# Kernel tuning notes

Hardware: AMD Instinct MI355X
Metric: run time of the kernel (lower is better)

The kernel has to match this reference:

```python
import jax, jax.numpy as jnp
import numpy as np

B, T, D, H = 2, 2048, 1024, 16
DH = D // H  # head_dim = 64
ROPE_BASE = 10000.0


def _rope_cos_sin(seq_len, dh, dtype):
    inv_freq = 1.0 / (ROPE_BASE ** (jnp.arange(0, dh, 2, dtype=jnp.float32) / dh))
    t = jnp.arange(seq_len, dtype=jnp.float32)
    freqs = jnp.outer(t, inv_freq)            # [T, dh/2]
    emb = jnp.concatenate([freqs, freqs], -1)  # [T, dh]
    return jnp.cos(emb).astype(dtype), jnp.sin(emb).astype(dtype)


def _rotate_half(x):
    half = x.shape[-1] // 2
    return jnp.concatenate([-x[..., half:], x[..., :half]], axis=-1)


def setup_inputs() -> dict:
    key = jax.random.key(0)
    k1, k2, k3 = jax.random.split(key, 3)
    x = jax.random.normal(k1, (B, T, D), dtype=jnp.float32)
    w_qkv = jax.random.normal(k2, (D, 3 * D), dtype=jnp.float32) * (D ** -0.5)
    w_out = jax.random.normal(k3, (D, D), dtype=jnp.float32) * (D ** -0.5)
    return {"x": x, "w_qkv": w_qkv, "w_out": w_out}


def reference(x, w_qkv, w_out):
    b, t, _ = x.shape
    qkv = x @ w_qkv                                        # [B,T,3D]
    qkv = qkv.reshape(b, t, 3, H, DH).transpose(2, 0, 3, 1, 4)  # [3,B,H,T,DH]
    q, k, v = qkv[0], qkv[1], qkv[2]

    cos, sin = _rope_cos_sin(t, DH, x.dtype)               # [T,DH] each
    q = q * cos + _rotate_half(q) * sin
    k = k * cos + _rotate_half(k) * sin

    scale = DH ** -0.5
    scores = jnp.einsum('bhtd,bhsd->bhts', q, k) * scale   # [B,H,T,T]
    # dense additive causal mask (as in original module)
    neg = jnp.finfo(x.dtype).min
    causal = jnp.triu(jnp.ones((t, t), dtype=bool), k=1)
    scores = scores + jnp.where(causal, neg, jnp.zeros((), x.dtype))
    attn = jax.nn.softmax(scores, axis=-1)
    out = jnp.einsum('bhts,bhsd->bhtd', attn, v)           # [B,H,T,DH]
    out = out.transpose(0, 2, 1, 3).reshape(b, t, D)       # [B,T,D]
    return out @ w_out
```

## Files before the change

### kernel.cpp

```cpp
#include <hip/hip_runtime.h>

typedef __bf16 bf16x8 __attribute__((ext_vector_type(8)));
typedef float f32x4 __attribute__((ext_vector_type(4)));
typedef unsigned int u32x4 __attribute__((ext_vector_type(4)));
typedef unsigned int u32x2 __attribute__((ext_vector_type(2)));
typedef unsigned short u16;
typedef unsigned int u32;

#define BSZ 2
#define TSEQ 2048
#define DMODEL 1024
#define NHEAD 16
#define DHEAD 64

#define GLDS(gp, lp)                                                        \
  __builtin_amdgcn_global_load_lds(                                         \
      (const __attribute__((address_space(1))) void*)(gp),                  \
      (__attribute__((address_space(3))) void*)(lp), 16, 0, 0)

#define TRR(dst, base, OFF)                                                 \
  asm volatile("ds_read_b64_tr_b16 %0, %1 offset:" OFF                     \
               : "=v"(dst) : "v"(base) : "memory")

__device__ __forceinline__ u16 f2bf(float f) {
  return __builtin_bit_cast(u16, (__bf16)f);
}
__device__ __forceinline__ u32 pack2bf(float lo, float hi) {
  return (u32)f2bf(lo) | ((u32)f2bf(hi) << 16);
}
__device__ __forceinline__ float bf2f(u16 h) {
  return __builtin_bit_cast(float, (u32)h << 16);
}

__global__ void k_prep(const float* __restrict__ x, u16* __restrict__ xb,
                       const float* __restrict__ wqkv, u16* __restrict__ wqkvT,
                       const float* __restrict__ wout, u16* __restrict__ woutT,
                       float* __restrict__ cosT, float* __restrict__ sinT) {
  __shared__ float tile[64][65];
  int blk = blockIdx.x, tid = threadIdx.x;
  if (blk < 2048) {
    int i = blk * 256 + tid;
    const float4* f4 = (const float4*)x;
    float4 v0 = f4[i * 2], v1 = f4[i * 2 + 1];
    u32x4 o;
    o[0] = pack2bf(v0.x, v0.y); o[1] = pack2bf(v0.z, v0.w);
    o[2] = pack2bf(v1.x, v1.y); o[3] = pack2bf(v1.z, v1.w);
    ((u32x4*)xb)[i] = o;
  } else if (blk < 2816) {
    int idx = blk - 2048;
    int n0 = (idx % 48) * 64, k0 = (idx / 48) * 64;
    int tx = tid & 63, ty = tid >> 6;
#pragma unroll
    for (int i = ty; i < 64; i += 4)
      tile[i][tx] = wqkv[(size_t)(k0 + i) * 3072 + n0 + tx];
    __syncthreads();
#pragma unroll
    for (int i = ty; i < 64; i += 4)
      wqkvT[(size_t)(n0 + i) * 1024 + k0 + tx] = f2bf(tile[tx][i]);
  } else if (blk < 3072) {
    int idx = blk - 2816;
    int n0 = (idx % 16) * 64, k0 = (idx / 16) * 64;
    int tx = tid & 63, ty = tid >> 6;
#pragma unroll
    for (int i = ty; i < 64; i += 4)
      tile[i][tx] = wout[(size_t)(k0 + i) * 1024 + n0 + tx];
    __syncthreads();
#pragma unroll
    for (int i = ty; i < 64; i += 4)
      woutT[(size_t)(n0 + i) * 1024 + k0 + tx] = f2bf(tile[tx][i]);
  } else {
    int idx = (blk - 3072) * 256 + tid;
    int t = idx >> 5, f = idx & 31;
    float inv_freq = powf(10000.0f, -(float)(2 * f) / 64.0f);
    float ang = (float)t * inv_freq;
    float s, c;
    sincosf(ang, &s, &c);
    cosT[idx] = c;
    sinT[idx] = s;
  }
}

__global__ __launch_bounds__(256) void k_gemm_qkv(const u16* __restrict__ A,
                                                  const u16* __restrict__ Bt,
                                                  u16* __restrict__ Qh, u16* __restrict__ Kh,
                                                  u16* __restrict__ Vh,
                                                  const float* __restrict__ cosT,
                                                  const float* __restrict__ sinT) {
  const int K = DMODEL;
  __shared__ __align__(16) u16 a_lds[2][128][32];
  __shared__ __align__(16) u16 b_lds[2][128][32];
  int m0 = blockIdx.y * 128, n0 = blockIdx.x * 128;
  int tid = threadIdx.x;
  int w = tid >> 6, l = tid & 63, lr = l & 15, lg = l >> 4;
  int wr = (w >> 1) * 64, wc = (w & 1) * 64;
  int grow = l >> 2;
  int gcol = (l & 3) * 8;
  f32x4 acc[4][4] = {};

  const u16* a0 = A + (size_t)(m0 + w * 16 + grow) * K + gcol;
  const u16* a1 = A + (size_t)(m0 + (w + 4) * 16 + grow) * K + gcol;
  const u16* b0 = Bt + (size_t)(n0 + w * 16 + grow) * K + gcol;
  const u16* b1 = Bt + (size_t)(n0 + (w + 4) * 16 + grow) * K + gcol;

  int NT = K >> 5;
  GLDS(a0, &a_lds[0][w * 16][0]);
  GLDS(a1, &a_lds[0][(w + 4) * 16][0]);
  GLDS(b0, &b_lds[0][w * 16][0]);
  GLDS(b1, &b_lds[0][(w + 4) * 16][0]);

  for (int t = 0; t < NT; ++t) {
    int p = t & 1;
    if (t + 1 < NT) {
      int k0 = (t + 1) << 5;
      GLDS(a0 + k0, &a_lds[p ^ 1][w * 16][0]);
      GLDS(a1 + k0, &a_lds[p ^ 1][(w + 4) * 16][0]);
      GLDS(b0 + k0, &b_lds[p ^ 1][w * 16][0]);
      GLDS(b1 + k0, &b_lds[p ^ 1][(w + 4) * 16][0]);
      asm volatile("s_waitcnt vmcnt(4)" ::: "memory");
    } else {
      asm volatile("s_waitcnt vmcnt(0)" ::: "memory");
    }
    __builtin_amdgcn_s_barrier();
    __builtin_amdgcn_sched_barrier(0);
    bf16x8 af[4], bfv[4];
#pragma unroll
    for (int mt = 0; mt < 4; ++mt)
      af[mt] = __builtin_bit_cast(bf16x8, *(const u32x4*)&a_lds[p][wr + mt * 16 + lr][lg * 8]);
#pragma unroll
    for (int nt = 0; nt < 4; ++nt)
      bfv[nt] = __builtin_bit_cast(bf16x8, *(const u32x4*)&b_lds[p][wc + nt * 16 + lr][lg * 8]);
    __builtin_amdgcn_s_setprio(1);
#pragma unroll
    for (int mt = 0; mt < 4; ++mt)
#pragma unroll
      for (int nt = 0; nt < 4; ++nt)
        acc[mt][nt] = __builtin_amdgcn_mfma_f32_16x16x32_bf16(af[mt], bfv[nt], acc[mt][nt], 0, 0, 0);
    __builtin_amdgcn_s_setprio(0);
    __builtin_amdgcn_sched_barrier(0);
    __builtin_amdgcn_s_barrier();
  }

  int sec = n0 >> 10;
  int hcol = ((n0 + wc) & 1023) >> 6;
  u16* outp = (sec == 0) ? Qh : (sec == 1) ? Kh : Vh;
  float qscale = (sec == 0) ? 0.125f : 1.0f;
#pragma unroll
  for (int mt = 0; mt < 4; ++mt)
#pragma unroll
    for (int r = 0; r < 4; ++r) {
      int row = m0 + wr + mt * 16 + lg * 4 + r;
      int b = row >> 11, tt = row & 2047;
      size_t obase = ((size_t)((b * 16 + hcol) * 2048 + tt)) * 64;
      if (sec == 2) {
#pragma unroll
        for (int nt = 0; nt < 4; ++nt)
          outp[obase + nt * 16 + lr] = f2bf(acc[mt][nt][r]);
      } else {
        float c0 = cosT[tt * 32 + lr],      s0 = sinT[tt * 32 + lr];
        float c1 = cosT[tt * 32 + 16 + lr], s1 = sinT[tt * 32 + 16 + lr];
        float v0 = acc[mt][0][r], v1 = acc[mt][1][r];
        float v2 = acc[mt][2][r], v3 = acc[mt][3][r];
        outp[obase + lr]      = f2bf((v0 * c0 - v2 * s0) * qscale);
        outp[obase + 16 + lr] = f2bf((v1 * c1 - v3 * s1) * qscale);
        outp[obase + 32 + lr] = f2bf((v2 * c0 + v0 * s0) * qscale);
        outp[obase + 48 + lr] = f2bf((v3 * c1 + v1 * s1) * qscale);
      }
    }
}

__global__ __launch_bounds__(256) void k_gemm_out(const u16* __restrict__ A,
                                                  const u16* __restrict__ Bt,
                                                  float* __restrict__ C) {
  const int N = 1024, K = 1024;
  __shared__ __align__(16) u16 a_lds[2][128][32];
  __shared__ __align__(16) u16 b_lds[2][64][32];
  int m0 = blockIdx.y * 128, n0 = blockIdx.x * 64;
  int tid = threadIdx.x;
  int w = tid >> 6, l = tid & 63, lr = l & 15, lg = l >> 4;
  int wr = (w >> 1) * 64, wc = (w & 1) * 32;
  int grow = l >> 2;
  int gcol = (l & 3) * 8;
  f32x4 acc[4][2] = {};

  const u16* a0 = A + (size_t)(m0 + w * 16 + grow) * K + gcol;
  const u16* a1 = A + (size_t)(m0 + (w + 4) * 16 + grow) * K + gcol;
  const u16* b0 = Bt + (size_t)(n0 + w * 16 + grow) * K + gcol;

  int NT = K >> 5;
  GLDS(a0, &a_lds[0][w * 16][0]);
  GLDS(a1, &a_lds[0][(w + 4) * 16][0]);
  GLDS(b0, &b_lds[0][w * 16][0]);

  for (int t = 0; t < NT; ++t) {
    int p = t & 1;
    if (t + 1 < NT) {
      int k0 = (t + 1) << 5;
      GLDS(a0 + k0, &a_lds[p ^ 1][w * 16][0]);
      GLDS(a1 + k0, &a_lds[p ^ 1][(w + 4) * 16][0]);
      GLDS(b0 + k0, &b_lds[p ^ 1][w * 16][0]);
      asm volatile("s_waitcnt vmcnt(3)" ::: "memory");
    } else {
      asm volatile("s_waitcnt vmcnt(0)" ::: "memory");
    }
    __builtin_amdgcn_s_barrier();
    __builtin_amdgcn_sched_barrier(0);
    bf16x8 af[4], bfv[2];
#pragma unroll
    for (int mt = 0; mt < 4; ++mt)
      af[mt] = __builtin_bit_cast(bf16x8, *(const u32x4*)&a_lds[p][wr + mt * 16 + lr][lg * 8]);
#pragma unroll
    for (int nt = 0; nt < 2; ++nt)
      bfv[nt] = __builtin_bit_cast(bf16x8, *(const u32x4*)&b_lds[p][wc + nt * 16 + lr][lg * 8]);
    __builtin_amdgcn_s_setprio(1);
#pragma unroll
    for (int mt = 0; mt < 4; ++mt)
#pragma unroll
      for (int nt = 0; nt < 2; ++nt)
        acc[mt][nt] = __builtin_amdgcn_mfma_f32_16x16x32_bf16(af[mt], bfv[nt], acc[mt][nt], 0, 0, 0);
    __builtin_amdgcn_s_setprio(0);
    __builtin_amdgcn_sched_barrier(0);
    __builtin_amdgcn_s_barrier();
  }

#pragma unroll
  for (int mt = 0; mt < 4; ++mt)
#pragma unroll
    for (int nt = 0; nt < 2; ++nt)
#pragma unroll
      for (int r = 0; r < 4; ++r) {
        int row = m0 + wr + mt * 16 + lg * 4 + r;
        int col = n0 + wc + nt * 16 + lr;
        C[(size_t)row * N + col] = acc[mt][nt][r];
      }
}

__global__ __launch_bounds__(512) void k_flash(const u16* __restrict__ Qg, const u16* __restrict__ Kg,
                                               const u16* __restrict__ Vg, u16* __restrict__ O) {
  __shared__ __align__(16) u16 k_lds[2][64][72];
  __shared__ __align__(16) u16 vsub[2][4096];
  __shared__ __align__(16) u16 p_lds[8][16][68];
  int pp = blockIdx.x;
  int qb1 = 31 - pp, qb2 = pp;
  int bh = blockIdx.y;
  int b = bh >> 4, h = bh & 15;
  size_t hoff = (size_t)bh * TSEQ * DHEAD;
  int tid = threadIdx.x, w = tid >> 6, l = tid & 63, lr = l & 15, lg = l >> 4;
  int team = w >> 2, wt = w & 3;
  int qb_t = team ? qb2 : qb1;

  int srow = tid >> 3;
  int g8 = tid & 7;
  int sc8 = g8 * 8;
  u32 vtr0 = (u32)(uintptr_t)vsub + (u32)(lg * 1024 + lr * 8);

  const u16* kbase = Kg + hoff;
  const u16* vbase = Vg + hoff;

  const u16* qp = Qg + hoff + (size_t)(qb_t * 64 + wt * 16 + lr) * 64 + lg * 8;
  bf16x8 qf0 = __builtin_bit_cast(bf16x8, *(const u32x4*)qp);
  bf16x8 qf1 = __builtin_bit_cast(bf16x8, *(const u32x4*)(qp + 32));

  f32x4 acc[4] = {};
  float mrow[4] = {-1e30f, -1e30f, -1e30f, -1e30f};
  float lsum[4] = {0.f, 0.f, 0.f, 0.f};

  u32x4 kreg, vreg;
  kreg = *(const u32x4*)(kbase + (size_t)srow * 64 + sc8);
  vreg = *(const u32x4*)(vbase + (size_t)srow * 64 + sc8);

  for (int kv = 0; kv <= qb1; ++kv) {
    int cur = kv & 1;
    *(u32x4*)&k_lds[cur][srow][sc8] = kreg;
    int vo = ((srow >> 2) * 4 + (g8 >> 1)) * 64 + (srow & 3) * 16 + (g8 & 1) * 8;
    *(u32x4*)&vsub[cur][vo] = vreg;
    __syncthreads();
    if (kv < qb1) {
      int r = (kv + 1) * 64 + srow;
      kreg = *(const u32x4*)(kbase + (size_t)r * 64 + sc8);
      vreg = *(const u32x4*)(vbase + (size_t)r * 64 + sc8);
    }

    if (kv <= qb_t) {
      u32 vtr = vtr0 + (u32)(cur * 8192);
      f32x4 s[4];
      __builtin_amdgcn_s_setprio(1);
#pragma unroll
      for (int c = 0; c < 4; ++c) {
        const u16* kp2 = &k_lds[cur][c * 16 + lr][lg * 8];
        bf16x8 kf0 = __builtin_bit_cast(bf16x8, *(const u32x4*)kp2);
        bf16x8 kf1 = __builtin_bit_cast(bf16x8, *(const u32x4*)(kp2 + 32));
        f32x4 z = {};
        z = __builtin_amdgcn_mfma_f32_16x16x32_bf16(qf0, kf0, z, 0, 0, 0);
        s[c] = __builtin_amdgcn_mfma_f32_16x16x32_bf16(qf1, kf1, z, 0, 0, 0);
      }
      __builtin_amdgcn_s_setprio(0);
      if (kv == qb_t) {
#pragma unroll
        for (int c = 0; c < 4; ++c)
#pragma unroll
          for (int r = 0; r < 4; ++r)
            if (c * 16 + lr > wt * 16 + lg * 4 + r) s[c][r] = -1e30f;
      }

      float rmax[4];
#pragma unroll
      for (int r = 0; r < 4; ++r)
        rmax[r] = fmaxf(fmaxf(s[0][r], s[1][r]), fmaxf(s[2][r], s[3][r]));
#pragma unroll
      for (int mset = 1; mset <= 8; mset <<= 1)
#pragma unroll
        for (int r = 0; r < 4; ++r)
          rmax[r] = fmaxf(rmax[r], __shfl_xor(rmax[r], mset, 64));
      bool need = (rmax[0] > mrow[0] + 8.0f) | (rmax[1] > mrow[1] + 8.0f) |
                  (rmax[2] > mrow[2] + 8.0f) | (rmax[3] > mrow[3] + 8.0f);
      if (__any(need)) {
        float alpha[4];
#pragma unroll
        for (int r = 0; r < 4; ++r) {
          float mn = fmaxf(mrow[r], rmax[r]);
          alpha[r] = __expf(mrow[r] - mn);
          mrow[r] = mn;
          lsum[r] *= alpha[r];
        }
#pragma unroll
        for (int n = 0; n < 4; ++n)
#pragma unroll
          for (int r = 0; r < 4; ++r)
            acc[n][r] *= alpha[r];
      }
#pragma unroll
      for (int c = 0; c < 4; ++c)
#pragma unroll
        for (int r = 0; r < 4; ++r) {
          float pe = __expf(s[c][r] - mrow[r]);
          s[c][r] = pe;
          lsum[r] += pe;
        }

#pragma unroll
      for (int c = 0; c < 4; ++c)
#pragma unroll
        for (int r = 0; r < 4; ++r)
          p_lds[w][lg * 4 + r][c * 16 + lr] = f2bf(s[c][r]);
      bf16x8 pa0 = __builtin_bit_cast(bf16x8, *(const u32x4*)&p_lds[w][lr][lg * 8]);
      bf16x8 pa1 = __builtin_bit_cast(bf16x8, *(const u32x4*)&p_lds[w][lr][lg * 8 + 32]);

      {
        u32x2 t[8];
        TRR(t[0], vtr, "0");    TRR(t[1], vtr, "512");
        TRR(t[2], vtr, "4096"); TRR(t[3], vtr, "4608");
        TRR(t[4], vtr, "128");  TRR(t[5], vtr, "640");
        TRR(t[6], vtr, "4224"); TRR(t[7], vtr, "4736");
        asm volatile("s_waitcnt lgkmcnt(0)" ::: "memory");
        __builtin_amdgcn_sched_barrier(0);
        __builtin_amdgcn_s_setprio(1);
#pragma unroll
        for (int n2 = 0; n2 < 2; ++n2) {
          u32x4 vlo, vhi;
          vlo[0] = t[n2 * 4 + 0][0]; vlo[1] = t[n2 * 4 + 0][1];
          vlo[2] = t[n2 * 4 + 1][0]; vlo[3] = t[n2 * 4 + 1][1];
          vhi[0] = t[n2 * 4 + 2][0]; vhi[1] = t[n2 * 4 + 2][1];
          vhi[2] = t[n2 * 4 + 3][0]; vhi[3] = t[n2 * 4 + 3][1];
          acc[n2] = __builtin_amdgcn_mfma_f32_16x16x32_bf16(pa0, __builtin_bit_cast(bf16x8, vlo), acc[n2], 0, 0, 0);
          acc[n2] = __builtin_amdgcn_mfma_f32_16x16x32_bf16(pa1, __builtin_bit_cast(bf16x8, vhi), acc[n2], 0, 0, 0);
        }
        __builtin_amdgcn_s_setprio(0);
      }
      {
        u32x2 t[8];
        TRR(t[0], vtr, "256");  TRR(t[1], vtr, "768");
        TRR(t[2], vtr, "4352"); TRR(t[3], vtr, "4864");
        TRR(t[4], vtr, "384");  TRR(t[5], vtr, "896");
        TRR(t[6], vtr, "4480"); TRR(t[7], vtr, "4992");
        asm volatile("s_waitcnt lgkmcnt(0)" ::: "memory");
        __builtin_amdgcn_sched_barrier(0);
        __builtin_amdgcn_s_setprio(1);
#pragma unroll
        for (int n2 = 0; n2 < 2; ++n2) {
          int n = 2 + n2;
          u32x4 vlo, vhi;
          vlo[0] = t[n2 * 4 + 0][0]; vlo[1] = t[n2 * 4 + 0][1];
          vlo[2] = t[n2 * 4 + 1][0]; vlo[3] = t[n2 * 4 + 1][1];
          vhi[0] = t[n2 * 4 + 2][0]; vhi[1] = t[n2 * 4 + 2][1];
          vhi[2] = t[n2 * 4 + 3][0]; vhi[3] = t[n2 * 4 + 3][1];
          acc[n] = __builtin_amdgcn_mfma_f32_16x16x32_bf16(pa0, __builtin_bit_cast(bf16x8, vlo), acc[n], 0, 0, 0);
          acc[n] = __builtin_amdgcn_mfma_f32_16x16x32_bf16(pa1, __builtin_bit_cast(bf16x8, vhi), acc[n], 0, 0, 0);
        }
        __builtin_amdgcn_s_setprio(0);
      }
    }
  }

#pragma unroll
  for (int mset = 1; mset <= 8; mset <<= 1)
#pragma unroll
    for (int r = 0; r < 4; ++r)
      lsum[r] += __shfl_xor(lsum[r], mset, 64);
#pragma unroll
  for (int n = 0; n < 4; ++n)
#pragma unroll
    for (int r = 0; r < 4; ++r) {
      int t = qb_t * 64 + wt * 16 + lg * 4 + r;
      int dd = n * 16 + lr;
      O[(size_t)(b * TSEQ + t) * DMODEL + h * 64 + dd] = f2bf(acc[n][r] / lsum[r]);
    }
}

extern "C" void kernel_launch(void* const* d_in, const int* in_sizes, int n_in,
                              void* d_out, int out_size, void* d_ws, size_t ws_size,
                              hipStream_t stream) {
  const float* x     = (const float*)d_in[0];
  const float* w_qkv = (const float*)d_in[1];
  const float* w_out = (const float*)d_in[2];
  float* out = (float*)d_out;

  char* ws = (char*)d_ws;
  size_t off = 0;
  auto alloc = [&](size_t bytes) {
    char* p = ws + off;
    off += (bytes + 255) & ~(size_t)255;
    return p;
  };
  const size_t MT = (size_t)BSZ * TSEQ;
  u16* xb    = (u16*)alloc(MT * DMODEL * 2);
  u16* wqkvT = (u16*)alloc((size_t)3 * DMODEL * DMODEL * 2);
  u16* woutT = (u16*)alloc((size_t)DMODEL * DMODEL * 2);
  u16* Qh    = (u16*)alloc(MT * DMODEL * 2);
  u16* Kh    = (u16*)alloc(MT * DMODEL * 2);
  u16* Vh    = (u16*)alloc(MT * DMODEL * 2);
  u16* aout  = (u16*)alloc(MT * DMODEL * 2);
  float* cosT = (float*)alloc((size_t)TSEQ * 32 * 4);
  float* sinT = (float*)alloc((size_t)TSEQ * 32 * 4);
  if (ws_size < off) return;

  k_prep<<<3328, 256, 0, stream>>>(x, xb, w_qkv, wqkvT, w_out, woutT, cosT, sinT);
  k_gemm_qkv<<<dim3(24, 32), 256, 0, stream>>>(xb, wqkvT, Qh, Kh, Vh, cosT, sinT);
  k_flash<<<dim3(16, BSZ * NHEAD), 512, 0, stream>>>(Qh, Kh, Vh, aout);
  k_gemm_out<<<dim3(16, 32), 256, 0, stream>>>(aout, woutT, out);
}
```

Before: 199.3 us.

## Process 128-key tiles per iteration in flash attention instead of double-buffered 64

The flash attention loop now stages 128 K/V rows per iteration into a single LDS buffer (two 64-row halves) instead of double-buffering 64-row tiles. This halves the number of barriers and online-softmax max/rescale steps per key row, and handles causal masking on partial 128 tiles by computing only the needed 16-column groups. It drops the LDS double buffering and adds an extra barrier before the stores, so load/compute overlap relies only on register prefetch. It also raises register pressure from the 8-wide score array.

Result: slower. 309.4 us (+55.2%).

```diff
diff --git a/kernel.cpp b/kernel.cpp
--- a/kernel.cpp
+++ b/kernel.cpp
@@ -236,7 +236,7 @@
 
 __global__ __launch_bounds__(512) void k_flash(const u16* __restrict__ Qg, const u16* __restrict__ Kg,
                                                const u16* __restrict__ Vg, u16* __restrict__ O) {
-  __shared__ __align__(16) u16 k_lds[2][64][72];
+  __shared__ __align__(16) u16 k_lds[128][72];
   __shared__ __align__(16) u16 vsub[2][4096];
   __shared__ __align__(16) u16 p_lds[8][16][68];
   int pp = blockIdx.x;
@@ -264,87 +264,120 @@
   float mrow[4] = {-1e30f, -1e30f, -1e30f, -1e30f};
   float lsum[4] = {0.f, 0.f, 0.f, 0.f};
 
-  u32x4 kreg, vreg;
-  kreg = *(const u32x4*)(kbase + (size_t)srow * 64 + sc8);
-  vreg = *(const u32x4*)(vbase + (size_t)srow * 64 + sc8);
-
-  for (int kv = 0; kv <= qb1; ++kv) {
-    int cur = kv & 1;
-    *(u32x4*)&k_lds[cur][srow][sc8] = kreg;
-    int vo = ((srow >> 2) * 4 + (g8 >> 1)) * 64 + (srow & 3) * 16 + (g8 & 1) * 8;
-    *(u32x4*)&vsub[cur][vo] = vreg;
+  u32x4 kreg[2], vreg[2];
+#pragma unroll
+  for (int p = 0; p < 2; ++p) {
+    int r = srow + p * 64;
+    kreg[p] = *(const u32x4*)(kbase + (size_t)r * 64 + sc8);
+    vreg[p] = *(const u32x4*)(vbase + (size_t)r * 64 + sc8);
+  }
+
+  int nkv = (qb1 >> 1) + 1;
+  for (int kvt = 0; kvt < nkv; ++kvt) {
     __syncthreads();
-    if (kv < qb1) {
-      int r = (kv + 1) * 64 + srow;
-      kreg = *(const u32x4*)(kbase + (size_t)r * 64 + sc8);
-      vreg = *(const u32x4*)(vbase + (size_t)r * 64 + sc8);
-    }
-
-    if (kv <= qb_t) {
-      u32 vtr = vtr0 + (u32)(cur * 8192);
-      f32x4 s[4];
-      __builtin_amdgcn_s_setprio(1);
-#pragma unroll
-      for (int c = 0; c < 4; ++c) {
-        const u16* kp2 = &k_lds[cur][c * 16 + lr][lg * 8];
-        bf16x8 kf0 = __builtin_bit_cast(bf16x8, *(const u32x4*)kp2);
-        bf16x8 kf1 = __builtin_bit_cast(bf16x8, *(const u32x4*)(kp2 + 32));
-        f32x4 z = {};
-        z = __builtin_amdgcn_mfma_f32_16x16x32_bf16(qf0, kf0, z, 0, 0, 0);
-        s[c] = __builtin_amdgcn_mfma_f32_16x16x32_bf16(qf1, kf1, z, 0, 0, 0);
-      }
-      __builtin_amdgcn_s_setprio(0);
-      if (kv == qb_t) {
-#pragma unroll
-        for (int c = 0; c < 4; ++c)
-#pragma unroll
-          for (int r = 0; r < 4; ++r)
-            if (c * 16 + lr > wt * 16 + lg * 4 + r) s[c][r] = -1e30f;
-      }
-
-      float rmax[4];
+#pragma unroll
+    for (int p = 0; p < 2; ++p) {
+      int r = srow + p * 64;
+      *(u32x4*)&k_lds[r][sc8] = kreg[p];
+      int rr = r & 63;
+      int vo = (r >> 6) * 4096 + (rr >> 2) * 256 + (g8 >> 1) * 64 + (rr & 3) * 16 + (g8 & 1) * 8;
+      *(u32x4*)&vsub[0][vo] = vreg[p];
+    }
+    __syncthreads();
+    if (kvt + 1 < nkv) {
+#pragma unroll
+      for (int p = 0; p < 2; ++p) {
+        int r = (kvt + 1) * 128 + srow + p * 64;
+        kreg[p] = *(const u32x4*)(kbase + (size_t)r * 64 + sc8);
+        vreg[p] = *(const u32x4*)(vbase + (size_t)r * 64 + sc8);
+      }
+    }
+
+    if (kvt * 2 > qb_t) continue;
+
+    int ng = 8, mstart = 8;
+    if (kvt == (qb_t >> 1)) {
+      if (qb_t & 1) { ng = 8; mstart = 4; }
+      else          { ng = 4; mstart = 0; }
+    }
+
+    f32x4 s[8];
+    __builtin_amdgcn_s_setprio(1);
+#pragma unroll
+    for (int c = 0; c < 8; ++c) {
+      if (c >= ng) break;
+      const u16* kp2 = &k_lds[c * 16 + lr][lg * 8];
+      bf16x8 kf0 = __builtin_bit_cast(bf16x8, *(const u32x4*)kp2);
+      bf16x8 kf1 = __builtin_bit_cast(bf16x8, *(const u32x4*)(kp2 + 32));
+      f32x4 z = {};
+      z = __builtin_amdgcn_mfma_f32_16x16x32_bf16(qf0, kf0, z, 0, 0, 0);
+      s[c] = __builtin_amdgcn_mfma_f32_16x16x32_bf16(qf1, kf1, z, 0, 0, 0);
+    }
+    __builtin_amdgcn_s_setprio(0);
+    int rowin = (qb_t & 1) * 64 + wt * 16 + lg * 4;
+#pragma unroll
+    for (int c = 0; c < 8; ++c) {
+      if (c >= ng) break;
+      if (c >= mstart) {
+#pragma unroll
+        for (int r = 0; r < 4; ++r)
+          if (c * 16 + lr > rowin + r) s[c][r] = -1e30f;
+      }
+    }
+
+    float rmax[4];
+#pragma unroll
+    for (int r = 0; r < 4; ++r) rmax[r] = s[0][r];
+#pragma unroll
+    for (int c = 1; c < 8; ++c) {
+      if (c >= ng) break;
+#pragma unroll
+      for (int r = 0; r < 4; ++r) rmax[r] = fmaxf(rmax[r], s[c][r]);
+    }
+#pragma unroll
+    for (int mset = 1; mset <= 8; mset <<= 1)
 #pragma unroll
       for (int r = 0; r < 4; ++r)
-        rmax[r] = fmaxf(fmaxf(s[0][r], s[1][r]), fmaxf(s[2][r], s[3][r]));
-#pragma unroll
-      for (int mset = 1; mset <= 8; mset <<= 1)
+        rmax[r] = fmaxf(rmax[r], __shfl_xor(rmax[r], mset, 64));
+    bool need = (rmax[0] > mrow[0] + 8.0f) | (rmax[1] > mrow[1] + 8.0f) |
+                (rmax[2] > mrow[2] + 8.0f) | (rmax[3] > mrow[3] + 8.0f);
+    if (__any(need)) {
+      float alpha[4];
+#pragma unroll
+      for (int r = 0; r < 4; ++r) {
+        float mn = fmaxf(mrow[r], rmax[r]);
+        alpha[r] = __expf(mrow[r] - mn);
+        mrow[r] = mn;
+        lsum[r] *= alpha[r];
+      }
+#pragma unroll
+      for (int n = 0; n < 4; ++n)
 #pragma unroll
         for (int r = 0; r < 4; ++r)
-          rmax[r] = fmaxf(rmax[r], __shfl_xor(rmax[r], mset, 64));
-      bool need = (rmax[0] > mrow[0] + 8.0f) | (rmax[1] > mrow[1] + 8.0f) |
-                  (rmax[2] > mrow[2] + 8.0f) | (rmax[3] > mrow[3] + 8.0f);
-      if (__any(need)) {
-        float alpha[4];
-#pragma unroll
-        for (int r = 0; r < 4; ++r) {
-          float mn = fmaxf(mrow[r], rmax[r]);
-          alpha[r] = __expf(mrow[r] - mn);
-          mrow[r] = mn;
-          lsum[r] *= alpha[r];
-        }
-#pragma unroll
-        for (int n = 0; n < 4; ++n)
-#pragma unroll
-          for (int r = 0; r < 4; ++r)
-            acc[n][r] *= alpha[r];
-      }
+          acc[n][r] *= alpha[r];
+    }
+#pragma unroll
+    for (int c = 0; c < 8; ++c) {
+      if (c >= ng) break;
+#pragma unroll
+      for (int r = 0; r < 4; ++r) {
+        float pe = __expf(s[c][r] - mrow[r]);
+        s[c][r] = pe;
+        lsum[r] += pe;
+      }
+    }
+
+#pragma unroll
+    for (int half = 0; half < 2; ++half) {
+      if (half == 1 && ng == 4) break;
 #pragma unroll
       for (int c = 0; c < 4; ++c)
 #pragma unroll
-        for (int r = 0; r < 4; ++r) {
-          float pe = __expf(s[c][r] - mrow[r]);
-          s[c][r] = pe;
-          lsum[r] += pe;
-        }
-
-#pragma unroll
-      for (int c = 0; c < 4; ++c)
-#pragma unroll
         for (int r = 0; r < 4; ++r)
-          p_lds[w][lg * 4 + r][c * 16 + lr] = f2bf(s[c][r]);
+          p_lds[w][lg * 4 + r][c * 16 + lr] = f2bf(s[half * 4 + c][r]);
       bf16x8 pa0 = __builtin_bit_cast(bf16x8, *(const u32x4*)&p_lds[w][lr][lg * 8]);
       bf16x8 pa1 = __builtin_bit_cast(bf16x8, *(const u32x4*)&p_lds[w][lr][lg * 8 + 32]);
-
+      u32 vtr = vtr0 + (u32)(half * 8192);
       {
         u32x2 t[8];
         TRR(t[0], vtr, "0");    TRR(t[1], vtr, "512");
```
